# Kernel tuning notes

Measured on AMD Instinct MI355X. Metric: run time of the kernel, lower is better.

The kernel has to match this reference:

```python
import jax, jax.numpy as jnp
import numpy as np

B, C, H, W = 2, 64, 128, 128
K, SCALE, NUM_RES = 3, 2, 2
KK = K * K


def conv(x, w, b, pad=0):
    y = jax.lax.conv_general_dilated(x, w, (1, 1), [(pad, pad), (pad, pad)],
                                     dimension_numbers=('NCHW', 'OIHW', 'NCHW'))
    return y + b[None, :, None, None]


def unfold_dilated(x, k, d):
    # mimics nn.Unfold(kernel_size=k, dilation=d, padding=(k//2)*d) -> (b, c, k*k, h, w)
    pad = (k // 2) * d
    b, c, h, w = x.shape
    xp = jnp.pad(x, ((0, 0), (0, 0), (pad, pad), (pad, pad)))
    slices = [xp[:, :, i * d:i * d + h, j * d:j * d + w]
              for i in range(k) for j in range(k)]
    return jnp.stack(slices, axis=2)


def setup_inputs() -> dict:
    key = jax.random.key(0)
    ks = jax.random.split(key, 32)
    def p(k, shape, s=0.05):
        return jax.random.normal(k, shape, dtype=jnp.float32) * s
    H2, W2 = H * SCALE, W * SCALE
    return {
        'depth':  p(ks[0], (B, C, H2, W2), 1.0),
        'guide':  p(ks[1], (B, C, H2, W2), 1.0),
        'inputs': p(ks[2], (B, C, H, W), 1.0),
        # depth_kernel branch: 1x1 C->C (ReLU), 1x1 C->k^2
        'dk_w1': p(ks[3], (C, C, 1, 1)), 'dk_b1': jnp.zeros((C,), jnp.float32),
        'dk_w2': p(ks[4], (KK, C, 1, 1)), 'dk_b2': jnp.zeros((KK,), jnp.float32),
        # guide_kernel branch
        'gk_w1': p(ks[5], (C, C, 1, 1)), 'gk_b1': jnp.zeros((C,), jnp.float32),
        'gk_w2': p(ks[6], (KK, C, 1, 1)), 'gk_b2': jnp.zeros((KK,), jnp.float32),
        # weight_net: 3x3 2C->C (ReLU), 3x3 C->C (ReLU, TUnet stand-in), 3x3 C->1
        'wn_w1': p(ks[7], (C, 2 * C, 3, 3)), 'wn_b1': jnp.zeros((C,), jnp.float32),
        'wn_w2': p(ks[8], (C, C, 3, 3)), 'wn_b2': jnp.zeros((C,), jnp.float32),
        'wn_w3': p(ks[9], (1, C, 3, 3)), 'wn_b3': jnp.zeros((1,), jnp.float32),
        # residual blocks on inputs: NUM_RES x (conv3x3-ReLU-conv3x3 + skip)
        'rb_w': p(ks[10], (NUM_RES, 2, C, C, 3, 3)),
        'rb_b': jnp.zeros((NUM_RES, 2, C), jnp.float32),
        'aff_scale': 0.5 * KK * jnp.ones((1,), jnp.float32),
    }


def reference(depth, guide, inputs,
              dk_w1, dk_b1, dk_w2, dk_b2,
              gk_w1, gk_b1, gk_w2, gk_b2,
              wn_w1, wn_b1, wn_w2, wn_b2, wn_w3, wn_b3,
              rb_w, rb_b, aff_scale):
    # weight map
    wm = jax.nn.relu(conv(jnp.concatenate([depth, guide], axis=1), wn_w1, wn_b1, 1))
    wm = jax.nn.relu(conv(wm, wn_w2, wn_b2, 1))
    weight_map = conv(wm, wn_w3, wn_b3, 1)                       # (b,1,h_,w_)
    # per-pixel kernels
    dk = conv(jax.nn.relu(conv(depth, dk_w1, dk_b1)), dk_w2, dk_b2)
    gk = conv(jax.nn.relu(conv(guide, gk_w1, gk_b1)), gk_w2, gk_b2)
    dk = jax.nn.softmax(dk, axis=1)
    gk = jax.nn.softmax(gk, axis=1)
    fuse = weight_map * dk + (1.0 - weight_map) * gk
    fuse = jnp.tanh(fuse) / (aff_scale + 1e-8)
    ksum = jnp.maximum(jnp.sum(jnp.abs(fuse), axis=1, keepdims=True) + 1e-4, 1.0)
    fuse = fuse / ksum                                            # (b,k^2,h_,w_)
    # residual conv stack on low-res inputs
    x = inputs
    for i in range(NUM_RES):
        r = jax.nn.relu(conv(x, rb_w[i, 0], rb_b[i, 0], 1))
        r = conv(r, rb_w[i, 1], rb_b[i, 1], 1)
        x = x + r
    b, c, h, w = x.shape
    up = jax.image.resize(x, (b, c, h * SCALE, w * SCALE), method='bilinear')
    unf = unfold_dilated(up, K, SCALE)                            # (b,c,k^2,h_,w_)
    out = jnp.einsum('bkhw,bckhw->bchw', fuse, unf)
    return out
```

## Files before the change

kernel.cpp:

```cpp
#include <hip/hip_runtime.h>
#include <hip/hip_bf16.h>
#include <math.h>

#define HW2 (256*256)
#define HW1 (128*128)

typedef __attribute__((ext_vector_type(8))) short short8;
typedef __attribute__((ext_vector_type(4))) float floatx4;

__device__ __forceinline__ float b2f(ushort u) {
    union { unsigned int i; float f; } v; v.i = ((unsigned int)u) << 16; return v.f;
}
__device__ __forceinline__ ushort f2b(float f) {
    __hip_bfloat16 h = __float2bfloat16(f); return *(ushort*)&h;
}

__global__ __launch_bounds__(256)
void repack_all(const float* __restrict__ wn_w1, const float* __restrict__ wn_w2,
                const float* __restrict__ rb_w,
                const float* __restrict__ dk_w1, const float* __restrict__ gk_w1,
                const float* __restrict__ dk_w2, const float* __restrict__ gk_w2,
                const float* __restrict__ wn_w3,
                ushort* __restrict__ wt_wn1, ushort* __restrict__ wt_wn2,
                ushort* __restrict__ wt_rb,
                ushort* __restrict__ w1d, ushort* __restrict__ w1g,
                ushort* __restrict__ w2d, ushort* __restrict__ w2g,
                ushort* __restrict__ wt3) {
    int idx = blockIdx.x * 256 + threadIdx.x;
    int role = blockIdx.y;
    if (role == 0) {
        if (idx >= 73728) return;
        int o = idx / 1152; int rem = idx - o * 1152;
        int ci = rem / 9;   int t = rem - ci * 9;
        wt_wn1[(((size_t)(ci >> 5) * 9 + t) * 64 + o) * 32 + (ci & 31)] = f2b(wn_w1[idx]);
    } else if (role <= 5) {
        if (idx >= 36864) return;
        const float* w = (role == 1) ? wn_w2 : rb_w + (size_t)(role - 2) * 36864;
        ushort* wt     = (role == 1) ? wt_wn2 : wt_rb + (size_t)(role - 2) * 36864;
        int o = idx / 576; int rem = idx - o * 576;
        int ci = rem / 9;  int t = rem - ci * 9;
        wt[(((size_t)(ci >> 5) * 9 + t) * 64 + o) * 32 + (ci & 31)] = f2b(w[idx]);
    } else if (role == 6) {
        if (idx >= 10240) return;
        if (idx < 4096)      w1d[idx] = f2b(dk_w1[idx]);
        else if (idx < 8192) w1g[idx - 4096] = f2b(gk_w1[idx - 4096]);
        else if (idx < 9216) { int i = idx - 8192; w2d[i] = (i >> 6) < 9 ? f2b(dk_w2[i]) : (ushort)0; }
        else                 { int i = idx - 9216; w2g[i] = (i >> 6) < 9 ? f2b(gk_w2[i]) : (ushort)0; }
    } else {
        if (idx >= 9216) return;
        int kc = idx / 512; int rem = idx - kc * 512;
        int n = rem >> 5, c = rem & 31;
        int cc = kc / 9, t = kc - cc * 9;
        wt3[idx] = (n == 0) ? f2b(wn_w3[(cc * 32 + c) * 9 + t]) : (ushort)0;
    }
}

__global__ __launch_bounds__(256)
void to_chunked(const float* __restrict__ in, ushort* __restrict__ outc,
                int H, int W, int Cchunks) {
    int P = W + 2, Q = H + 2;
    int plane_px = P * Q;
    int idx = blockIdx.x * 256 + threadIdx.x;
    if (idx >= plane_px) return;
    int py = idx / P, px = idx - py * P;
    int bc = blockIdx.y;
    int b = bc / Cchunks, cc = bc - b * Cchunks;
    ushort* dst = outc + ((size_t)bc * plane_px + idx) * 32;
    if (py == 0 || py == Q - 1 || px == 0 || px == P - 1) {
        for (int c = 0; c < 32; ++c) dst[c] = 0;
        return;
    }
    int y = py - 1, x = px - 1;
    const float* src = in + ((size_t)b * (Cchunks * 32) + cc * 32) * H * W
                          + (size_t)y * W + x;
    for (int c = 0; c < 32; ++c)
        dst[c] = f2b(src[(size_t)c * H * W]);
}

__global__ __launch_bounds__(256)
void to_chunked_hi(const float* __restrict__ depth, const float* __restrict__ guide,
                   ushort* __restrict__ outc) {
    const int P = 258;
    int plane_px = P * P;
    int idx = blockIdx.x * 256 + threadIdx.x;
    if (idx >= plane_px) return;
    int py = idx / P, px = idx - py * P;
    int pl = blockIdx.y;
    const float* srcb = (pl < 4) ? depth : guide;
    int bc = pl & 3;
    int b = bc >> 1, cc = bc & 1;
    ushort* dst = outc + ((size_t)pl * plane_px + idx) * 32;
    if (py == 0 || py == P - 1 || px == 0 || px == P - 1) {
        for (int c = 0; c < 32; ++c) dst[c] = 0;
        return;
    }
    int y = py - 1, x = px - 1;
    const float* src = srcb + ((size_t)b * 64 + cc * 32) * HW2 + (size_t)y * 256 + x;
    for (int c = 0; c < 32; ++c)
        dst[c] = f2b(src[(size_t)c * HW2]);
}

__global__ __launch_bounds__(256)
void zero_border2(ushort* __restrict__ buf256, ushort* __restrict__ buf128) {
    int region = blockIdx.y;
    int H = region ? 128 : 256;
    int P = H + 2, Q = H + 2;
    ushort* buf = region ? buf128 : buf256;
    int nb = 2 * P + 2 * H;
    int idx = blockIdx.x * 256 + threadIdx.x;
    if (idx >= nb * 8) return;
    int pl = idx / nb, r = idx - pl * nb;
    int py, px;
    if (r < P)          { py = 0;     px = r; }
    else if (r < 2 * P) { py = Q - 1; px = r - P; }
    else { int k = r - 2 * P; py = 1 + (k >> 1); px = (k & 1) ? P - 1 : 0; }
    ushort* dst = buf + ((size_t)pl * P * Q + (size_t)py * P + px) * 32;
    for (int c = 0; c < 32; ++c) dst[c] = 0;
}

template<int NCHUNK, int ROWS, bool RELU, bool HAS_SKIP, bool CONCAT2>
__global__ __launch_bounds__(256)
void conv3x3_reg(const ushort* __restrict__ inA, const ushort* __restrict__ inB,
                 const ushort* __restrict__ wt, const float* __restrict__ bias,
                 const ushort* __restrict__ skip, ushort* __restrict__ outc,
                 int H, int W) {
    const int P = W + 2;
    const size_t plane = (size_t)P * (H + 2) * 32;
    int tid = threadIdx.x;
    int wv = tid >> 6, lane = tid & 63, ml = lane & 15, q = lane >> 4;
    int x0 = blockIdx.x * 16;
    int rowsPerBlock = (blockDim.x >> 6) * ROWS;
    int yb = blockIdx.y * rowsPerBlock + wv * ROWS;
    int b = blockIdx.z;

    floatx4 acc[ROWS][4];
#pragma unroll
    for (int r = 0; r < ROWS; ++r)
#pragma unroll
        for (int n = 0; n < 4; ++n) acc[r][n] = (floatx4){0.f, 0.f, 0.f, 0.f};

    for (int cc = 0; cc < NCHUNK; ++cc) {
        const ushort* base;
        if (CONCAT2) {
            constexpr int HC = NCHUNK / 2;
            if (cc < HC) base = inA + ((size_t)(b * HC + cc)) * plane;
            else         base = inB + ((size_t)(b * HC + cc - HC)) * plane;
        } else {
            base = inA + ((size_t)(b * NCHUNK + cc)) * plane;
        }
        const ushort* wb = wt + (size_t)cc * 18432;
#pragma unroll
        for (int t = 0; t < 9; ++t) {
            int dy = t / 3, dx = t - 3 * dy;
            short8 afr[ROWS], bfr[4];
#pragma unroll
            for (int r = 0; r < ROWS; ++r)
                afr[r] = *(const short8*)&base[((size_t)(yb + r + dy) * P
                                               + (x0 + ml + dx)) * 32 + q * 8];
#pragma unroll
            for (int n = 0; n < 4; ++n)
                bfr[n] = *(const short8*)&wb[(size_t)(t * 64 + n * 16 + ml) * 32 + q * 8];
#pragma unroll
            for (int r = 0; r < ROWS; ++r)
#pragma unroll
                for (int n = 0; n < 4; ++n)
                    acc[r][n] = __builtin_amdgcn_mfma_f32_16x16x32_bf16(
                        afr[r], bfr[n], acc[r][n], 0, 0, 0);
        }
    }

#pragma unroll
    for (int r = 0; r < ROWS; ++r) {
        int y = yb + r;
#pragma unroll
        for (int n = 0; n < 4; ++n) {
            int ch = n * 16 + ml;
            int occ = ch >> 5, ocl = ch & 31;
            float bs = bias[ch];
            size_t pbase = ((size_t)(b * 2 + occ)) * plane + ((size_t)(y + 1) * P) * 32 + ocl;
#pragma unroll
            for (int e = 0; e < 4; ++e) {
                int x = x0 + q * 4 + e;
                float v = acc[r][n][e] + bs;
                if (RELU) v = fmaxf(v, 0.f);
                if (HAS_SKIP)
                    v += b2f(skip[((size_t)(b * 2 + occ)) * plane
                                  + ((size_t)(y + 1) * P + (x + 1)) * 32 + ocl]);
                outc[pbase + (size_t)(x + 1) * 32] = f2b(v);
            }
        }
    }
}

__global__ __launch_bounds__(256)
void kernels_fuse_mfma(const ushort* __restrict__ depth_c, const ushort* __restrict__ guide_c,
                       const ushort* __restrict__ bufB,
                       const ushort* __restrict__ wt3, const float* __restrict__ wn_b3,
                       const ushort* __restrict__ w1d, const float* __restrict__ b1d,
                       const ushort* __restrict__ w2d, const float* __restrict__ b2d,
                       const ushort* __restrict__ w1g, const float* __restrict__ b1g,
                       const ushort* __restrict__ w2g, const float* __restrict__ b2g,
                       const float* __restrict__ aff, float* __restrict__ fuse_out) {
    __shared__ __align__(16) ushort hid[2][4][16 * 72];
    __shared__ float wmv[4][16];

    int tid = threadIdx.x;
    int wv = tid >> 6, lane = tid & 63, ml = lane & 15, q = lane >> 4;
    int p0 = blockIdx.x * 64 + wv * 16;
    int b = p0 >> 16, rem0 = p0 & 65535;
    const size_t plane = (size_t)258 * 258 * 32;

    int rem = rem0 + ml;
    int y = rem >> 8, x = rem & 255;
    size_t poff = ((size_t)(y + 1) * 258 + (x + 1)) * 32;

    floatx4 dwm = (floatx4){0.f, 0.f, 0.f, 0.f};
#pragma unroll
    for (int cc = 0; cc < 2; ++cc) {
        const ushort* basep = bufB + (size_t)(b * 2 + cc) * plane;
#pragma unroll
        for (int t = 0; t < 9; ++t) {
            int dy = t / 3, dx = t - 3 * dy;
            short8 a3 = *(const short8*)&basep[((size_t)(y + dy) * 258 + (x + dx)) * 32 + q * 8];
            short8 b3 = *(const short8*)&wt3[(size_t)((cc * 9 + t) * 512 + ml * 32 + q * 8)];
            dwm = __builtin_amdgcn_mfma_f32_16x16x32_bf16(a3, b3, dwm, 0, 0, 0);
        }
    }
    if (ml == 0) {
#pragma unroll
        for (int e = 0; e < 4; ++e) wmv[wv][q * 4 + e] = dwm[e];
    }
    float wm = wmv[wv][ml] + wn_b3[0];

    float sm[2][4];
    for (int br = 0; br < 2; ++br) {
        const ushort* src = br ? guide_c : depth_c;
        const ushort* w1  = br ? w1g : w1d;
        const float*  b1  = br ? b1g : b1d;
        const ushort* w2  = br ? w2g : w2d;
        const float*  b2  = br ? b2g : b2d;
        ushort* h = hid[br][wv];

        short8 afr[2];
#pragma unroll
        for (int kc = 0; kc < 2; ++kc)
            afr[kc] = *(const short8*)&src[(size_t)(b * 2 + kc) * plane + poff + q * 8];

        floatx4 acc[4];
#pragma unroll
        for (int nt = 0; nt < 4; ++nt) acc[nt] = (floatx4){0.f, 0.f, 0.f, 0.f};
#pragma unroll
        for (int nt = 0; nt < 4; ++nt)
#pragma unroll
            for (int kc = 0; kc < 2; ++kc) {
                short8 bfr = *(const short8*)&w1[(size_t)((nt * 16 + ml) * 64 + kc * 32 + q * 8)];
                acc[nt] = __builtin_amdgcn_mfma_f32_16x16x32_bf16(afr[kc], bfr, acc[nt], 0, 0, 0);
            }

#pragma unroll
        for (int nt = 0; nt < 4; ++nt) {
            float bs = b1[nt * 16 + ml];
#pragma unroll
            for (int e = 0; e < 4; ++e) {
                float v = acc[nt][e] + bs;
                v = fmaxf(v, 0.f);
                h[(q * 4 + e) * 72 + nt * 16 + ml] = f2b(v);
            }
        }

        floatx4 d2 = (floatx4){0.f, 0.f, 0.f, 0.f};
#pragma unroll
        for (int kc = 0; kc < 2; ++kc) {
            short8 a2 = *(const short8*)&w2[(size_t)(ml * 64 + kc * 32 + q * 8)];
            short8 hf = *(const short8*)&h[ml * 72 + kc * 32 + q * 8];
            d2 = __builtin_amdgcn_mfma_f32_16x16x32_bf16(a2, hf, d2, 0, 0, 0);
        }

        float lg[4];
#pragma unroll
        for (int e = 0; e < 4; ++e) {
            int j = q * 4 + e;
            lg[e] = (j < 9) ? (d2[e] + b2[j]) : -1e30f;
        }
        float m = fmaxf(fmaxf(lg[0], lg[1]), fmaxf(lg[2], lg[3]));
        m = fmaxf(m, __shfl_xor(m, 16));
        m = fmaxf(m, __shfl_xor(m, 32));
        float s = 0.f;
#pragma unroll
        for (int e = 0; e < 4; ++e) { lg[e] = __expf(lg[e] - m); s += lg[e]; }
        s += __shfl_xor(s, 16);
        s += __shfl_xor(s, 32);
        float inv = 1.f / s;
#pragma unroll
        for (int e = 0; e < 4; ++e) sm[br][e] = lg[e] * inv;
    }

    float inv_av = 1.f / (aff[0] + 1e-8f);
    float f[4];
    float s = 0.f;
#pragma unroll
    for (int e = 0; e < 4; ++e) {
        float v = wm * sm[0][e] + (1.f - wm) * sm[1][e];
        v = tanhf(v) * inv_av;
        f[e] = v;
        s += fabsf(v);
    }
    s += __shfl_xor(s, 16);
    s += __shfl_xor(s, 32);
    float ksum = s + 1e-4f;
    if (ksum < 1.f) ksum = 1.f;
    float invk = 1.f / ksum;
#pragma unroll
    for (int e = 0; e < 4; ++e) {
        int j = q * 4 + e;
        if (j < 9)
            fuse_out[((size_t)b * 9 + j) * HW2 + rem0 + ml] = f[e] * invk;
    }
}

__global__ __launch_bounds__(256)
void fuse_apply_up(const float* __restrict__ fuse, const ushort* __restrict__ r2c,
                   float* __restrict__ out) {
    int p = blockIdx.x * 256 + threadIdx.x;
    int pl = blockIdx.y;
    int b = pl >> 1, cc = pl & 1;
    int y = p >> 8, x = p & 255;

    int my = y >> 1, mx = x >> 1;
    float wyA = (y & 1) ? 0.75f : 0.25f;  float wyB = 1.f - wyA;
    float wxA = (x & 1) ? 0.75f : 0.25f;  float wxB = 1.f - wxA;
    int R0y = my + ((y & 1) ? 0 : -1) - 1;
    int R0x = mx + ((x & 1) ? 0 : -1) - 1;

    const float* f = fuse + (size_t)b * 9 * HW2 + p;
    float coef[4][4];
#pragma unroll
    for (int k = 0; k < 4; ++k)
#pragma unroll
        for (int l = 0; l < 4; ++l) coef[k][l] = 0.f;

#pragma unroll
    for (int ty = 0; ty < 3; ++ty) {
        int yp = y + (ty - 1) * 2;
        if (yp < 0 || yp > 255) continue;
#pragma unroll
        for (int tx = 0; tx < 3; ++tx) {
            int xp = x + (tx - 1) * 2;
            if (xp < 0 || xp > 255) continue;
            float fv = f[(size_t)(ty * 3 + tx) * HW2];
            coef[ty][tx]         += fv * wyA * wxA;
            coef[ty][tx + 1]     += fv * wyA * wxB;
            coef[ty + 1][tx]     += fv * wyB * wxA;
            coef[ty + 1][tx + 1] += fv * wyB * wxB;
        }
    }

    const ushort* base = r2c + (size_t)pl * 130 * 130 * 32;
    float acc[32];
#pragma unroll
    for (int c = 0; c < 32; ++c) acc[c] = 0.f;
#pragma unroll
    for (int k = 0; k < 4; ++k) {
        int ry = R0y + k; ry = ry < 0 ? 0 : (ry > 127 ? 127 : ry);
#pragma unroll
        for (int l = 0; l < 4; ++l) {
            int rx = R0x + l; rx = rx < 0 ? 0 : (rx > 127 ? 127 : rx);
            float cf = coef[k][l];
            const ushort* u = base + ((size_t)(ry + 1) * 130 + (rx + 1)) * 32;
#pragma unroll
            for (int c = 0; c < 32; ++c) acc[c] = fmaf(cf, b2f(u[c]), acc[c]);
        }
    }
    float* ob = out + ((size_t)(b * 64 + cc * 32)) * HW2 + p;
#pragma unroll
    for (int c = 0; c < 32; ++c) ob[(size_t)c * HW2] = acc[c];
}

extern "C" void kernel_launch(void* const* d_in, const int* in_sizes, int n_in,
                              void* d_out, int out_size, void* d_ws, size_t ws_size,
                              hipStream_t stream) {
    const float* depth  = (const float*)d_in[0];
    const float* guide  = (const float*)d_in[1];
    const float* inputs = (const float*)d_in[2];
    const float* dk_w1  = (const float*)d_in[3];
    const float* dk_b1  = (const float*)d_in[4];
    const float* dk_w2  = (const float*)d_in[5];
    const float* dk_b2  = (const float*)d_in[6];
    const float* gk_w1  = (const float*)d_in[7];
    const float* gk_b1  = (const float*)d_in[8];
    const float* gk_w2  = (const float*)d_in[9];
    const float* gk_b2  = (const float*)d_in[10];
    const float* wn_w1  = (const float*)d_in[11];
    const float* wn_b1  = (const float*)d_in[12];
    const float* wn_w2  = (const float*)d_in[13];
    const float* wn_b2  = (const float*)d_in[14];
    const float* wn_w3  = (const float*)d_in[15];
    const float* wn_b3  = (const float*)d_in[16];
    const float* rb_w   = (const float*)d_in[17];
    const float* rb_b   = (const float*)d_in[18];
    const float* aff    = (const float*)d_in[19];
    float* out = (float*)d_out;

    float* ws = (float*)d_ws;
    size_t off = 0;
    const size_t CH256 = 4260096;
    const size_t CH128 = 1081600;
    ushort* depth_c = (ushort*)(ws + off); off += CH256;
    ushort* guide_c = (ushort*)(ws + off); off += CH256;
    ushort* bufA    = (ushort*)(ws + off); off += CH256;
    ushort* bufB    = (ushort*)(ws + off); off += CH256;
    ushort* inp_c   = (ushort*)(ws + off); off += CH128;
    ushort* r0      = (ushort*)(ws + off); off += CH128;
    ushort* r1      = (ushort*)(ws + off); off += CH128;
    ushort* r2      = (ushort*)(ws + off); off += CH128;
    float* fuse     = ws + off; off += 1179648;
    ushort* wt_wn1  = (ushort*)(ws + off); off += 36864;
    ushort* wt_wn2  = (ushort*)(ws + off); off += 18432;
    ushort* wt_rb   = (ushort*)(ws + off); off += 73728;
    ushort* w1d_b   = (ushort*)(ws + off); off += 2048;
    ushort* w1g_b   = (ushort*)(ws + off); off += 2048;
    ushort* w2d_b   = (ushort*)(ws + off); off += 512;
    ushort* w2g_b   = (ushort*)(ws + off); off += 512;
    ushort* wt3_b   = (ushort*)(ws + off); off += 4608;

    repack_all<<<dim3(288, 8), 256, 0, stream>>>(
        wn_w1, wn_w2, rb_w, dk_w1, gk_w1, dk_w2, gk_w2, wn_w3,
        wt_wn1, wt_wn2, wt_rb, w1d_b, w1g_b, w2d_b, w2g_b, wt3_b);

    to_chunked_hi<<<dim3(261, 8), 256, 0, stream>>>(depth, guide, depth_c);
    to_chunked<<<dim3(67, 4), 256, 0, stream>>>(inputs, inp_c, 128, 128, 2);

    zero_border2<<<dim3(33, 2), 256, 0, stream>>>(bufA, r0);

    conv3x3_reg<4, 4, true, false, true ><<<dim3(16, 16, 2), 256, 0, stream>>>(
        depth_c, guide_c, wt_wn1, wn_b1, nullptr, bufA, 256, 256);
    conv3x3_reg<2, 4, true, false, false><<<dim3(16, 16, 2), 256, 0, stream>>>(
        bufA, nullptr, wt_wn2, wn_b2, nullptr, bufB, 256, 256);

    kernels_fuse_mfma<<<2048, 256, 0, stream>>>(depth_c, guide_c, bufB,
                                                wt3_b, wn_b3,
                                                w1d_b, dk_b1, w2d_b, dk_b2,
                                                w1g_b, gk_b1, w2g_b, gk_b2,
                                                aff, fuse);

    conv3x3_reg<2, 2, true,  false, false><<<dim3(8, 16, 2), 256, 0, stream>>>(
        inp_c, nullptr, wt_rb + 0 * 36864, rb_b + 0 * 64, nullptr, r0, 128, 128);
    conv3x3_reg<2, 2, false, true,  false><<<dim3(8, 16, 2), 256, 0, stream>>>(
        r0, nullptr, wt_rb + 1 * 36864, rb_b + 1 * 64, inp_c, r1, 128, 128);
    conv3x3_reg<2, 2, true,  false, false><<<dim3(8, 16, 2), 256, 0, stream>>>(
        r1, nullptr, wt_rb + 2 * 36864, rb_b + 2 * 64, nullptr, r0, 128, 128);
    conv3x3_reg<2, 2, false, true,  false><<<dim3(8, 16, 2), 256, 0, stream>>>(
        r0, nullptr, wt_rb + 3 * 36864, rb_b + 3 * 64, r1, r2, 128, 128);

    fuse_apply_up<<<dim3(256, 4), 256, 0, stream>>>(fuse, r2, out);
}
```

Baseline: 329.4 us.

## Merge independent branches into shared launches to cut kernel count

Folds the three layout-prep and border-zeroing kernels into a single prep kernel. Each low-res residual conv is co-launched with an independent high-res stage (wn conv1, wn conv2, kernel fusion) by dispatching on blockIdx.z. The high-res convs also drop from 4 to 2 rows per wave, which doubles their block count. The aim is to remove launch gaps and let the small 128x128 convs fill idle CUs next to the large ones. In exchange there is some branch overhead, idle early-exit blocks in the padded grids, and less per-wave reuse in the high-res convs.

```diff
diff --git a/kernel.cpp b/kernel.cpp
--- a/kernel.cpp
+++ b/kernel.cpp
@@ -56,82 +56,67 @@
 }
 
 __global__ __launch_bounds__(256)
-void to_chunked(const float* __restrict__ in, ushort* __restrict__ outc,
-                int H, int W, int Cchunks) {
-    int P = W + 2, Q = H + 2;
-    int plane_px = P * Q;
+void prep_act(const float* __restrict__ depth, const float* __restrict__ guide,
+              const float* __restrict__ inputs,
+              ushort* __restrict__ dg_c, ushort* __restrict__ inp_c,
+              ushort* __restrict__ buf256, ushort* __restrict__ buf128) {
+    int role = blockIdx.y;
     int idx = blockIdx.x * 256 + threadIdx.x;
-    if (idx >= plane_px) return;
-    int py = idx / P, px = idx - py * P;
-    int bc = blockIdx.y;
-    int b = bc / Cchunks, cc = bc - b * Cchunks;
-    ushort* dst = outc + ((size_t)bc * plane_px + idx) * 32;
-    if (py == 0 || py == Q - 1 || px == 0 || px == P - 1) {
+    if (role < 8) {
+        const int P = 258;
+        if (idx >= P * P) return;
+        int py = idx / P, px = idx - py * P;
+        const float* srcb = (role < 4) ? depth : guide;
+        int bc = role & 3;
+        int b = bc >> 1, cc = bc & 1;
+        ushort* dst = dg_c + ((size_t)role * P * P + idx) * 32;
+        if (py == 0 || py == P - 1 || px == 0 || px == P - 1) {
+            for (int c = 0; c < 32; ++c) dst[c] = 0;
+            return;
+        }
+        int y = py - 1, x = px - 1;
+        const float* src = srcb + ((size_t)b * 64 + cc * 32) * HW2 + (size_t)y * 256 + x;
+        for (int c = 0; c < 32; ++c) dst[c] = f2b(src[(size_t)c * HW2]);
+    } else if (role == 8) {
+        const int P = 130;
+        if (idx >= 4 * P * P) return;
+        int pl = idx / (P * P), p = idx - pl * (P * P);
+        int py = p / P, px = p - py * P;
+        int b = pl >> 1, cc = pl & 1;
+        ushort* dst = inp_c + ((size_t)pl * P * P + p) * 32;
+        if (py == 0 || py == P - 1 || px == 0 || px == P - 1) {
+            for (int c = 0; c < 32; ++c) dst[c] = 0;
+            return;
+        }
+        int y = py - 1, x = px - 1;
+        const float* src = inputs + ((size_t)b * 64 + cc * 32) * HW1 + (size_t)y * 128 + x;
+        for (int c = 0; c < 32; ++c) dst[c] = f2b(src[(size_t)c * HW1]);
+    } else {
+        if (idx >= 12352) return;
+        ushort* buf; int P, H, pl, r;
+        if (idx < 8224) { P = 258; H = 256; buf = buf256; pl = idx / 1028; r = idx - pl * 1028; }
+        else { int k = idx - 8224; P = 130; H = 128; buf = buf128; pl = k / 516; r = k - pl * 516; }
+        int py, px;
+        if (r < P)          { py = 0;     px = r; }
+        else if (r < 2 * P) { py = P - 1; px = r - P; }
+        else { int k = r - 2 * P; py = 1 + (k >> 1); px = (k & 1) ? P - 1 : 0; }
+        ushort* dst = buf + ((size_t)pl * P * P + (size_t)py * P + px) * 32;
         for (int c = 0; c < 32; ++c) dst[c] = 0;
-        return;
-    }
-    int y = py - 1, x = px - 1;
-    const float* src = in + ((size_t)b * (Cchunks * 32) + cc * 32) * H * W
-                          + (size_t)y * W + x;
-    for (int c = 0; c < 32; ++c)
-        dst[c] = f2b(src[(size_t)c * H * W]);
-}
-
-__global__ __launch_bounds__(256)
-void to_chunked_hi(const float* __restrict__ depth, const float* __restrict__ guide,
-                   ushort* __restrict__ outc) {
-    const int P = 258;
-    int plane_px = P * P;
-    int idx = blockIdx.x * 256 + threadIdx.x;
-    if (idx >= plane_px) return;
-    int py = idx / P, px = idx - py * P;
-    int pl = blockIdx.y;
-    const float* srcb = (pl < 4) ? depth : guide;
-    int bc = pl & 3;
-    int b = bc >> 1, cc = bc & 1;
-    ushort* dst = outc + ((size_t)pl * plane_px + idx) * 32;
-    if (py == 0 || py == P - 1 || px == 0 || px == P - 1) {
-        for (int c = 0; c < 32; ++c) dst[c] = 0;
-        return;
-    }
-    int y = py - 1, x = px - 1;
-    const float* src = srcb + ((size_t)b * 64 + cc * 32) * HW2 + (size_t)y * 256 + x;
-    for (int c = 0; c < 32; ++c)
-        dst[c] = f2b(src[(size_t)c * HW2]);
-}
-
-__global__ __launch_bounds__(256)
-void zero_border2(ushort* __restrict__ buf256, ushort* __restrict__ buf128) {
-    int region = blockIdx.y;
-    int H = region ? 128 : 256;
-    int P = H + 2, Q = H + 2;
-    ushort* buf = region ? buf128 : buf256;
-    int nb = 2 * P + 2 * H;
-    int idx = blockIdx.x * 256 + threadIdx.x;
-    if (idx >= nb * 8) return;
-    int pl = idx / nb, r = idx - pl * nb;
-    int py, px;
-    if (r < P)          { py = 0;     px = r; }
-    else if (r < 2 * P) { py = Q - 1; px = r - P; }
-    else { int k = r - 2 * P; py = 1 + (k >> 1); px = (k & 1) ? P - 1 : 0; }
-    ushort* dst = buf + ((size_t)pl * P * Q + (size_t)py * P + px) * 32;
-    for (int c = 0; c < 32; ++c) dst[c] = 0;
+    }
 }
 
 template<int NCHUNK, int ROWS, bool RELU, bool HAS_SKIP, bool CONCAT2>
-__global__ __launch_bounds__(256)
-void conv3x3_reg(const ushort* __restrict__ inA, const ushort* __restrict__ inB,
-                 const ushort* __restrict__ wt, const float* __restrict__ bias,
-                 const ushort* __restrict__ skip, ushort* __restrict__ outc,
-                 int H, int W) {
+__device__ __forceinline__
+void conv3x3_body(const ushort* __restrict__ inA, const ushort* __restrict__ inB,
+                  const ushort* __restrict__ wt, const float* __restrict__ bias,
+                  const ushort* __restrict__ skip, ushort* __restrict__ outc,
+                  int H, int W, int bx, int by, int b) {
     const int P = W + 2;
     const size_t plane = (size_t)P * (H + 2) * 32;
     int tid = threadIdx.x;
     int wv = tid >> 6, lane = tid & 63, ml = lane & 15, q = lane >> 4;
-    int x0 = blockIdx.x * 16;
-    int rowsPerBlock = (blockDim.x >> 6) * ROWS;
-    int yb = blockIdx.y * rowsPerBlock + wv * ROWS;
-    int b = blockIdx.z;
+    int x0 = bx * 16;
+    int yb = by * (4 * ROWS) + wv * ROWS;
 
     floatx4 acc[ROWS][4];
 #pragma unroll
@@ -192,21 +177,68 @@
     }
 }
 
-__global__ __launch_bounds__(256)
-void kernels_fuse_mfma(const ushort* __restrict__ depth_c, const ushort* __restrict__ guide_c,
-                       const ushort* __restrict__ bufB,
-                       const ushort* __restrict__ wt3, const float* __restrict__ wn_b3,
-                       const ushort* __restrict__ w1d, const float* __restrict__ b1d,
-                       const ushort* __restrict__ w2d, const float* __restrict__ b2d,
-                       const ushort* __restrict__ w1g, const float* __restrict__ b1g,
-                       const ushort* __restrict__ w2g, const float* __restrict__ b2g,
-                       const float* __restrict__ aff, float* __restrict__ fuse_out) {
-    __shared__ __align__(16) ushort hid[2][4][16 * 72];
-    __shared__ float wmv[4][16];
-
+template<int NCHUNK, int ROWS, bool RELU, bool HAS_SKIP, bool CONCAT2>
+__global__ __launch_bounds__(256)
+void conv3x3_k(const ushort* __restrict__ inA, const ushort* __restrict__ inB,
+               const ushort* __restrict__ wt, const float* __restrict__ bias,
+               const ushort* __restrict__ skip, ushort* __restrict__ outc,
+               int H, int W) {
+    conv3x3_body<NCHUNK, ROWS, RELU, HAS_SKIP, CONCAT2>(
+        inA, inB, wt, bias, skip, outc, H, W, blockIdx.x, blockIdx.y, blockIdx.z);
+}
+
+__global__ __launch_bounds__(256)
+void convA(const ushort* __restrict__ depth_c, const ushort* __restrict__ guide_c,
+           const ushort* __restrict__ wt_wn1, const float* __restrict__ wn_b1,
+           ushort* __restrict__ bufA,
+           const ushort* __restrict__ inp_c, const ushort* __restrict__ wt_rb0,
+           const float* __restrict__ rb_b0, ushort* __restrict__ r0) {
+    int z = blockIdx.z;
+    if (z < 2) {
+        conv3x3_body<4, 2, true, false, true>(depth_c, guide_c, wt_wn1, wn_b1,
+                                              nullptr, bufA, 256, 256,
+                                              blockIdx.x, blockIdx.y, z);
+    } else {
+        if (blockIdx.x >= 8 || blockIdx.y >= 16) return;
+        conv3x3_body<2, 2, true, false, false>(inp_c, nullptr, wt_rb0, rb_b0,
+                                               nullptr, r0, 128, 128,
+                                               blockIdx.x, blockIdx.y, z - 2);
+    }
+}
+
+__global__ __launch_bounds__(256)
+void convB(const ushort* __restrict__ bufA, const ushort* __restrict__ wt_wn2,
+           const float* __restrict__ wn_b2, ushort* __restrict__ bufB,
+           const ushort* __restrict__ r0, const ushort* __restrict__ wt_rb1,
+           const float* __restrict__ rb_b1, const ushort* __restrict__ inp_c,
+           ushort* __restrict__ r1) {
+    int z = blockIdx.z;
+    if (z < 2) {
+        conv3x3_body<2, 2, true, false, false>(bufA, nullptr, wt_wn2, wn_b2,
+                                               nullptr, bufB, 256, 256,
+                                               blockIdx.x, blockIdx.y, z);
+    } else {
+        if (blockIdx.x >= 8 || blockIdx.y >= 16) return;
+        conv3x3_body<2, 2, false, true, false>(r0, nullptr, wt_rb1, rb_b1,
+                                               inp_c, r1, 128, 128,
+                                               blockIdx.x, blockIdx.y, z - 2);
+    }
+}
+
+__device__ __forceinline__
+void fuse_body(ushort* __restrict__ hid, float* __restrict__ wmv,
+               const ushort* __restrict__ depth_c, const ushort* __restrict__ guide_c,
+               const ushort* __restrict__ bufB,
+               const ushort* __restrict__ wt3, const float* __restrict__ wn_b3,
+               const ushort* __restrict__ w1d, const float* __restrict__ b1d,
+               const ushort* __restrict__ w2d, const float* __restrict__ b2d,
+               const ushort* __restrict__ w1g, const float* __restrict__ b1g,
+               const ushort* __restrict__ w2g, const float* __restrict__ b2g,
+               const float* __restrict__ aff, float* __restrict__ fuse_out,
+               int bx) {
     int tid = threadIdx.x;
     int wv = tid >> 6, lane = tid & 63, ml = lane & 15, q = lane >> 4;
-    int p0 = blockIdx.x * 64 + wv * 16;
+    int p0 = bx * 64 + wv * 16;
     int b = p0 >> 16, rem0 = p0 & 65535;
     const size_t plane = (size_t)258 * 258 * 32;
 
@@ -228,9 +260,9 @@
     }
     if (ml == 0) {
 #pragma unroll
-        for (int e = 0; e < 4; ++e) wmv[wv][q * 4 + e] = dwm[e];
-    }
-    float wm = wmv[wv][ml] + wn_b3[0];
+        for (int e = 0; e < 4; ++e) wmv[wv * 16 + q * 4 + e] = dwm[e];
+    }
+    float wm = wmv[wv * 16 + ml] + wn_b3[0];
 
     float sm[2][4];
     for (int br = 0; br < 2; ++br) {
@@ -239,7 +271,7 @@
         const float*  b1  = br ? b1g : b1d;
         const ushort* w2  = br ? w2g : w2d;
         const float*  b2  = br ? b2g : b2d;
-        ushort* h = hid[br][wv];
+        ushort* h = hid + (size_t)(br * 4 + wv) * (16 * 72);
 
         short8 afr[2];
 #pragma unroll
@@ -315,6 +347,32 @@
         int j = q * 4 + e;
         if (j < 9)
             fuse_out[((size_t)b * 9 + j) * HW2 + rem0 + ml] = f[e] * invk;
+    }
+}
+
+__global__ __launch_bounds__(256)
+void fuse_rb2(const ushort* __restrict__ depth_c, const ushort* __restrict__ guide_c,
+              const ushort* __restrict__ bufB,
+              const ushort* __restrict__ wt3, const float* __restrict__ wn_b3,
+              const ushort* __restrict__ w1d, const float* __restrict__ b1d,
+              const ushort* __restrict__ w2d, const float* __restrict__ b2d,
+              const ushort* __restrict__ w1g, const float* __restrict__ b1g,
+              const ushort* __restrict__ w2g, const float* __restrict__ b2g,
+              const float* __restrict__ aff, float* __restrict__ fuse_out,
+              const ushort* __restrict__ r1, const ushort* __restrict__ wt_rb2,
+              const float* __restrict__ rb_b2, ushort* __restrict__ r0) {
+    __shared__ __align__(16) ushort hid[2 * 4 * 16 * 72];
+    __shared__ float wmv[4 * 16];
+    int z = blockIdx.z;
+    if (z == 0) {
+        fuse_body(hid, wmv, depth_c, guide_c, bufB, wt3, wn_b3,
+                  w1d, b1d, w2d, b2d, w1g, b1g, w2g, b2g,
+                  aff, fuse_out, blockIdx.x);
+    } else {
+        if (blockIdx.x >= 128) return;
+        conv3x3_body<2, 2, true, false, false>(r1, nullptr, wt_rb2, rb_b2,
+                                               nullptr, r0, 128, 128,
+                                               blockIdx.x & 7, blockIdx.x >> 3, z - 1);
     }
 }
 
@@ -426,30 +484,24 @@
     repack_all<<<dim3(288, 8), 256, 0, stream>>>(
         wn_w1, wn_w2, rb_w, dk_w1, gk_w1, dk_w2, gk_w2, wn_w3,
         wt_wn1, wt_wn2, wt_rb, w1d_b, w1g_b, w2d_b, w2g_b, wt3_b);
-
-    to_chunked_hi<<<dim3(261, 8), 256, 0, stream>>>(depth, guide, depth_c);
-    to_chunked<<<dim3(67, 4), 256, 0, stream>>>(inputs, inp_c, 128, 128, 2);
-
-    zero_border2<<<dim3(33, 2), 256, 0, stream>>>(bufA, r0);
-
-    conv3x3_reg<4, 4, true, false, true ><<<dim3(16, 16, 2), 256, 0, stream>>>(
-        depth_c, guide_c, wt_wn1, wn_b1, nullptr, bufA, 256, 256);
-    conv3x3_reg<2, 4, true, false, false><<<dim3(16, 16, 2), 256, 0, stream>>>(
-        bufA, nullptr, wt_wn2, wn_b2, nullptr, bufB, 256, 256);
-
-    kernels_fuse_mfma<<<2048, 256, 0, stream>>>(depth_c, guide_c, bufB,
-                                                wt3_b, wn_b3,
-                                                w1d_b, dk_b1, w2d_b, dk_b2,
-                                                w1g_b, gk_b1, w2g_b, gk_b2,
-                                                aff, fuse);
-
-    conv3x3_reg<2, 2, true,  false, false><<<dim3(8, 16, 2), 256, 0, stream>>>(
-        inp_c, nullptr, wt_rb + 0 * 36864, rb_b + 0 * 64, nullptr, r0, 128, 128);
-    conv3x3_reg<2, 2, false, true,  false><<<dim3(8, 16, 2), 256, 0, stream>>>(
-        r0, nullptr, wt_rb + 1 * 36864, rb_b + 1 * 64, inp_c, r1, 128, 128);
-    conv3x3_reg<2, 2, true,  false, false><<<dim3(8, 16, 2), 256, 0, stream>>>(
-        r1, nullptr, wt_rb + 2 * 36864, rb_b + 2 * 64, nullptr, r0, 128, 128);
-    conv3x3_reg<2, 2, false, true,  false><<<dim3(8, 16, 2), 256, 0, stream>>>(
+    prep_act<<<dim3(265, 10), 256, 0, stream>>>(
+        depth, guide, inputs, depth_c, inp_c, bufA, r0);
+
+    convA<<<dim3(16, 32, 4), 256, 0, stream>>>(
+        depth_c, guide_c, wt_wn1, wn_b1, bufA,
+        inp_c, wt_rb + 0 * 36864, rb_b + 0 * 64, r0);
+
+    convB<<<dim3(16, 32, 4), 256, 0, stream>>>(
+        bufA, wt_wn2, wn_b2, bufB,
+        r0, wt_rb + 1 * 36864, rb_b + 1 * 64, inp_c, r1);
+
+    fuse_rb2<<<dim3(2048, 1, 3), 256, 0, stream>>>(
+        depth_c, guide_c, bufB, wt3_b, wn_b3,
+        w1d_b, dk_b1, w2d_b, dk_b2, w1g_b, gk_b1, w2g_b, gk_b2,
+        aff, fuse,
+        r1, wt_rb + 2 * 36864, rb_b + 2 * 64, r0);
+
+    conv3x3_k<2, 2, false, true, false><<<dim3(8, 16, 2), 256, 0, stream>>>(
         r0, nullptr, wt_rb + 3 * 36864, rb_b + 3 * 64, r1, r2, 128, 128);
 
     fuse_apply_up<<<dim3(256, 4), 256, 0, stream>>>(fuse, r2, out);
```

After: 349.8 us. 1.06x slower.
